# Kernel tuning notes

Measured on AMD Instinct MI355X. Metric: run time of the kernel, lower is better.

The kernel has to match this reference:

```python
import jax, jax.numpy as jnp
import numpy as np

NEG_SLOPE = 0.2
LN_EPS = 1e-5


def gat_conv(x, src, dst, n_nodes, W, a_src, a_dst, b, concat):
    # W: [F_in, H*C]; a_src, a_dst: [H, C]; b: [H*C] if concat else [C]
    H, C = a_src.shape
    h = (x @ W).reshape(-1, H, C)                      # [N, H, C]
    # per-node attention scores, gathered per edge
    s_src = jnp.einsum('nhc,hc->nh', h, a_src)          # [N, H]
    s_dst = jnp.einsum('nhc,hc->nh', h, a_dst)          # [N, H]
    e = jax.nn.leaky_relu(s_src[src] + s_dst[dst], NEG_SLOPE)  # [E, H]
    # segment softmax over incoming edges of each dst node
    e_max = jax.ops.segment_max(e, dst, num_segments=n_nodes)  # [N, H]
    w = jnp.exp(e - e_max[dst])
    denom = jax.ops.segment_sum(w, dst, num_segments=n_nodes)
    alpha = w / (denom[dst] + 1e-16)                    # [E, H]
    # weighted scatter-aggregate of source messages
    msg = h[src] * alpha[:, :, None]                    # [E, H, C]
    out = jax.ops.segment_sum(msg, dst, num_segments=n_nodes)  # [N, H, C]
    out = out.reshape(n_nodes, H * C) if concat else out.mean(axis=1)
    return out + b


def layer_norm(x, g, b):
    mu = x.mean(-1, keepdims=True)
    var = ((x - mu) ** 2).mean(-1, keepdims=True)
    return (x - mu) * jax.lax.rsqrt(var + LN_EPS) * g + b


def setup_inputs() -> dict:
    key = jax.random.key(0)
    ks = jax.random.split(key, 16)
    N, E, F_in = 50000, 400000, 128
    H1, C1 = 4, 128          # conv1: heads=4, hidden=128, concat -> 512
    C2 = 64                  # conv2: heads=1, out=64
    sd = lambda fan: 1.0 / np.sqrt(fan)
    inp = {
        'x': jax.random.normal(ks[0], (N, F_in), jnp.float32),
        'edge_index': jax.random.randint(ks[1], (2, E), 0, N, jnp.int64),
        'num_nodes': N,
        'W1': jax.random.normal(ks[2], (F_in, H1 * C1), jnp.float32) * sd(F_in),
        'a_src1': jax.random.normal(ks[3], (H1, C1), jnp.float32) * sd(C1),
        'a_dst1': jax.random.normal(ks[4], (H1, C1), jnp.float32) * sd(C1),
        'b1': jnp.zeros((H1 * C1,), jnp.float32),
        'W2': jax.random.normal(ks[5], (H1 * C1, C2), jnp.float32) * sd(H1 * C1),
        'a_src2': jax.random.normal(ks[6], (1, C2), jnp.float32) * sd(C2),
        'a_dst2': jax.random.normal(ks[7], (1, C2), jnp.float32) * sd(C2),
        'b2': jnp.zeros((C2,), jnp.float32),
        'Wm1': jax.random.normal(ks[8], (C2, 32), jnp.float32) * sd(C2),
        'bm1': jnp.zeros((32,), jnp.float32),
        'g_ln': jnp.ones((32,), jnp.float32),
        'b_ln': jnp.zeros((32,), jnp.float32),
        'Wm2': jax.random.normal(ks[9], (32, 16), jnp.float32) * sd(32),
        'bm2': jnp.zeros((16,), jnp.float32),
    }
    return inp


def reference(x, edge_index, num_nodes, W1, a_src1, a_dst1, b1, W2, a_src2, a_dst2, b2, Wm1, bm1, g_ln, b_ln, Wm2, bm2):
    N = num_nodes
    # PyG GATConv add_self_loops=True
    loop = jnp.arange(N, dtype=edge_index.dtype)
    src = jnp.concatenate([edge_index[0], loop])
    dst = jnp.concatenate([edge_index[1], loop])
    # dropout layers are identity in eval mode
    h = jax.nn.elu(gat_conv(x, src, dst, N, W1, a_src1, a_dst1, b1, concat=True))
    h = jax.nn.elu(gat_conv(h, src, dst, N, W2, a_src2, a_dst2, b2, concat=False))
    h = jax.nn.relu(layer_norm(h @ Wm1 + bm1, g_ln, b_ln))
    return h @ Wm2 + bm2  # [N, 2*n_spectral_dims]
```

## Files before the change

### kernel.cpp

```cpp
#include <hip/hip_runtime.h>
#include <cmath>


#define F_IN 128
#define H1   4
#define C1   128
#define D1   512
#define C2   64
#define DM1  32
#define DM2  16

#define LRELU(x) ((x) > 0.f ? (x) : 0.2f * (x))

typedef float f32x4 __attribute__((ext_vector_type(4)));
typedef short short8 __attribute__((ext_vector_type(8)));

static __device__ __forceinline__ float bf2f(unsigned short u) {
    return __builtin_bit_cast(float, (unsigned)u << 16);
}
static __device__ __forceinline__ unsigned short f2bf(float f) {
    unsigned u = __builtin_bit_cast(unsigned, f);
    u = (u + 0x7fffu + ((u >> 16) & 1u)) >> 16;
    return (unsigned short)u;
}

__global__ void k_detect(const void* ei, int E, int* flag) {
    __shared__ int any;
    if (threadIdx.x == 0) any = 0;
    __syncthreads();
    const int* p = (const int*)ei;
    int cnt = E < 4096 ? E : 4096;
    int stride = E / cnt;
    int local = 0;
    for (int i = threadIdx.x; i < cnt; i += blockDim.x) {
        long long idx = (long long)i * stride;
        local |= p[2 * idx + 1];
    }
    if (local) atomicOr(&any, 1);
    __syncthreads();
    if (threadIdx.x == 0) *flag = (any == 0) ? 1 : 0;
}

__global__ void k_convert(const void* ei, const int* flag, int E, int N,
                          int* src32, int* dst32, int* deg) {
    int i = blockIdx.x * blockDim.x + threadIdx.x;
    int Etot = E + N;
    if (i >= Etot) return;
    int s, d;
    if (i < E) {
        if (*flag) {
            const long long* q = (const long long*)ei;
            s = (int)q[i];
            d = (int)q[(size_t)E + i];
        } else {
            const int* q = (const int*)ei;
            s = q[i];
            d = q[(size_t)E + i];
        }
    } else {
        s = i - E;
        d = i - E;
    }
    src32[i] = s;
    dst32[i] = d;
    atomicAdd(&deg[d], 1);
}

__global__ __launch_bounds__(256) void k_scan1(const int* __restrict__ deg,
                                               int* __restrict__ bsum, int N) {
    int t = threadIdx.x;
    int base = blockIdx.x * 1024 + t * 4;
    int s = 0;
    if (base + 3 < N) {
        int4 v = *(const int4*)&deg[base];
        s = v.x + v.y + v.z + v.w;
    } else {
        for (int k = 0; k < 4; k++)
            if (base + k < N) s += deg[base + k];
    }
#pragma unroll
    for (int o = 1; o < 64; o <<= 1) s += __shfl_xor(s, o, 64);
    __shared__ int ws[4];
    if ((t & 63) == 0) ws[t >> 6] = s;
    __syncthreads();
    if (t == 0) bsum[blockIdx.x] = ws[0] + ws[1] + ws[2] + ws[3];
}

__global__ __launch_bounds__(1024) void k_scan2(const int* __restrict__ bsum,
                                                int* __restrict__ boff, int nb) {
    __shared__ int wsum[16];
    __shared__ int woff[16];
    int t = threadIdx.x, lane = t & 63, wid = t >> 6;
    int v = (t < nb) ? bsum[t] : 0;
    int x = v;
#pragma unroll
    for (int o = 1; o < 64; o <<= 1) {
        int tv = __shfl_up(x, o, 64);
        if (lane >= o) x += tv;
    }
    if (lane == 63) wsum[wid] = x;
    __syncthreads();
    if (wid == 0) {
        int y = (lane < 16) ? wsum[lane] : 0;
        int z = y;
#pragma unroll
        for (int o = 1; o < 16; o <<= 1) {
            int tv = __shfl_up(z, o, 64);
            if (lane >= o) z += tv;
        }
        if (lane < 16) woff[lane] = z - y;
    }
    __syncthreads();
    if (t < nb) boff[t] = woff[wid] + x - v;
}

__global__ __launch_bounds__(256) void k_scan3(const int* __restrict__ deg,
                                               const int* __restrict__ boff,
                                               int* __restrict__ rowstart,
                                               int* __restrict__ cursor, int N,
                                               int Etot) {
    int t = threadIdx.x, lane = t & 63, wid = t >> 6;
    int base = blockIdx.x * 1024 + t * 4;
    int v0 = 0, v1 = 0, v2 = 0, v3 = 0;
    if (base + 3 < N) {
        int4 v = *(const int4*)&deg[base];
        v0 = v.x; v1 = v.y; v2 = v.z; v3 = v.w;
    } else {
        if (base + 0 < N) v0 = deg[base + 0];
        if (base + 1 < N) v1 = deg[base + 1];
        if (base + 2 < N) v2 = deg[base + 2];
        if (base + 3 < N) v3 = deg[base + 3];
    }
    int s4 = v0 + v1 + v2 + v3;
    int x = s4;
#pragma unroll
    for (int o = 1; o < 64; o <<= 1) {
        int tv = __shfl_up(x, o, 64);
        if (lane >= o) x += tv;
    }
    __shared__ int ws[4];
    if (lane == 63) ws[wid] = x;
    __syncthreads();
    int woff = 0;
#pragma unroll
    for (int w = 0; w < 4; w++)
        if (w < wid) woff += ws[w];
    int ex = boff[blockIdx.x] + woff + (x - s4);
    int e0 = ex, e1 = ex + v0, e2 = e1 + v1, e3 = e2 + v2;
    if (base + 0 < N) { rowstart[base + 0] = e0; cursor[base + 0] = e0; }
    if (base + 1 < N) { rowstart[base + 1] = e1; cursor[base + 1] = e1; }
    if (base + 2 < N) { rowstart[base + 2] = e2; cursor[base + 2] = e2; }
    if (base + 3 < N) { rowstart[base + 3] = e3; cursor[base + 3] = e3; }
    if (blockIdx.x == 0 && t == 0) rowstart[N] = Etot;
}

__global__ void k_fill(const int* __restrict__ src32, const int* __restrict__ dst32,
                       int* __restrict__ cursor, int* __restrict__ adj, int Etot) {
    int i = blockIdx.x * blockDim.x + threadIdx.x;
    if (i < Etot) {
        int d = dst32[i];
        int pos = atomicAdd(&cursor[d], 1);
        adj[pos] = src32[i];
    }
}

__global__ void k_prep(const float* __restrict__ x, const float* __restrict__ W1,
                       const float* __restrict__ W2,
                       unsigned short* __restrict__ xb,
                       unsigned short* __restrict__ W1t,
                       unsigned short* __restrict__ W2t, int n8) {
    int i = blockIdx.x * blockDim.x + threadIdx.x;
    if (i < n8) {
        const float4* p = (const float4*)(x + (size_t)i * 8);
        float4 a = p[0], b = p[1];
        unsigned short r[8] = {f2bf(a.x), f2bf(a.y), f2bf(a.z), f2bf(a.w),
                               f2bf(b.x), f2bf(b.y), f2bf(b.z), f2bf(b.w)};
        *(short8*)(xb + (size_t)i * 8) = *(const short8*)r;
        return;
    }
    int i2 = i - n8;
    if (i2 < F_IN * D1) {
        int nn = i2 / F_IN, kk = i2 - nn * F_IN;
        W1t[i2] = f2bf(W1[(size_t)kk * D1 + nn]);
        return;
    }
    int i3 = i2 - F_IN * D1;
    if (i3 < D1 * C2) {
        int nn = i3 / D1, kk = i3 - nn * D1;
        W2t[i3] = f2bf(W2[(size_t)kk * C2 + nn]);
    }
}

template <int WM, int WN, int MF, int NF, bool OUT_BF16>
__global__ __launch_bounds__(256) void k_gemm_bf16(
    const unsigned short* __restrict__ A, const unsigned short* __restrict__ Bt,
    void* __restrict__ C, int M, int K, int NC) {
    constexpr int BM = WM * MF * 16;
    constexpr int BN = WN * NF * 16;
    constexpr int BK = 64;
    constexpr int LDK = BK + 8;
    __shared__ unsigned short As[BM][LDK];
    __shared__ unsigned short Bs[BN][LDK];
    const int tid = threadIdx.x;
    const int row0 = blockIdx.x * BM, col0 = blockIdx.y * BN;
    const int wave = tid >> 6, lane = tid & 63;
    const int wr = wave / WN, wc = wave % WN;
    const int lrow = lane & 15, lkg = lane >> 4;
    f32x4 acc[MF][NF] = {};
    for (int k0 = 0; k0 < K; k0 += BK) {
        for (int i = tid; i < BM * BK / 8; i += 256) {
            int r = i >> 3, kq = (i & 7) * 8;
            short8 v = {};
            if (row0 + r < M)
                v = *(const short8*)&A[(size_t)(row0 + r) * K + k0 + kq];
            *(short8*)&As[r][kq] = v;
        }
        for (int i = tid; i < BN * BK / 8; i += 256) {
            int r = i >> 3, kq = (i & 7) * 8;
            short8 v = *(const short8*)&Bt[(size_t)(col0 + r) * K + k0 + kq];
            *(short8*)&Bs[r][kq] = v;
        }
        __syncthreads();
#pragma unroll
        for (int kk = 0; kk < BK; kk += 32) {
            short8 af[MF], bfr[NF];
#pragma unroll
            for (int m = 0; m < MF; m++)
                af[m] = *(const short8*)&As[wr * MF * 16 + m * 16 + lrow][kk + lkg * 8];
#pragma unroll
            for (int n = 0; n < NF; n++)
                bfr[n] = *(const short8*)&Bs[wc * NF * 16 + n * 16 + lrow][kk + lkg * 8];
#pragma unroll
            for (int m = 0; m < MF; m++)
#pragma unroll
                for (int n = 0; n < NF; n++)
                    acc[m][n] = __builtin_amdgcn_mfma_f32_16x16x32_bf16(
                        af[m], bfr[n], acc[m][n], 0, 0, 0);
        }
        __syncthreads();
    }
#pragma unroll
    for (int m = 0; m < MF; m++)
#pragma unroll
        for (int n = 0; n < NF; n++)
#pragma unroll
            for (int r = 0; r < 4; r++) {
                int gr = row0 + wr * MF * 16 + m * 16 + lkg * 4 + r;
                int gc = col0 + wc * NF * 16 + n * 16 + lrow;
                if (gr < M) {
                    if (OUT_BF16)
                        ((unsigned short*)C)[(size_t)gr * NC + gc] = f2bf(acc[m][n][r]);
                    else
                        ((float*)C)[(size_t)gr * NC + gc] = acc[m][n][r];
                }
            }
}

__global__ void k_scores1(const unsigned short* __restrict__ h1b,
                          const float* __restrict__ a_src,
                          const float* __restrict__ a_dst,
                          float* __restrict__ s_src, float* __restrict__ s_dst,
                          int N) {
    int gid = blockIdx.x * blockDim.x + threadIdx.x;
    int n = gid >> 6, lane = gid & 63;
    if (n >= N) return;
    short8 hv = *(const short8*)&h1b[(size_t)n * D1 + lane * 8];
    float h[8];
#pragma unroll
    for (int j = 0; j < 8; j++) h[j] = bf2f((unsigned short)hv[j]);
    const float4* ap = (const float4*)&a_src[lane * 8];
    float4 a0 = ap[0], a1 = ap[1];
    const float4* bp = (const float4*)&a_dst[lane * 8];
    float4 b0 = bp[0], b1v = bp[1];
    float ss = h[0] * a0.x + h[1] * a0.y + h[2] * a0.z + h[3] * a0.w +
               h[4] * a1.x + h[5] * a1.y + h[6] * a1.z + h[7] * a1.w;
    float dd = h[0] * b0.x + h[1] * b0.y + h[2] * b0.z + h[3] * b0.w +
               h[4] * b1v.x + h[5] * b1v.y + h[6] * b1v.z + h[7] * b1v.w;
#pragma unroll
    for (int o = 1; o < 16; o <<= 1) {
        ss += __shfl_xor(ss, o, 64);
        dd += __shfl_xor(dd, o, 64);
    }
    if ((lane & 15) == 0) {
        int h4 = lane >> 4;
        s_src[(size_t)n * H1 + h4] = ss;
        s_dst[(size_t)n * H1 + h4] = dd;
    }
}

__global__ void k_scores2(const float* __restrict__ h2lin,
                          const float* __restrict__ a_src,
                          const float* __restrict__ a_dst,
                          float* __restrict__ s_src, float* __restrict__ s_dst,
                          int N) {
    int gid = blockIdx.x * blockDim.x + threadIdx.x;
    int n = gid >> 6, lane = gid & 63;
    if (n >= N) return;
    float v = h2lin[(size_t)n * C2 + lane];
    float ss = v * a_src[lane], dd = v * a_dst[lane];
#pragma unroll
    for (int o = 1; o < 64; o <<= 1) {
        ss += __shfl_xor(ss, o, 64);
        dd += __shfl_xor(dd, o, 64);
    }
    if (lane == 0) {
        s_src[n] = ss;
        s_dst[n] = dd;
    }
}

__global__ __launch_bounds__(256) void k_agg1(
    const unsigned short* __restrict__ h1b, const float* __restrict__ s_src,
    const float* __restrict__ s_dst, const int* __restrict__ rowstart,
    const int* __restrict__ adj, const float* __restrict__ b1,
    unsigned short* __restrict__ out1, int N) {
    int wv = (blockIdx.x * blockDim.x + threadIdx.x) >> 6;
    if (wv >= N) return;
    int lane = threadIdx.x & 63;
    int beg = rowstart[wv], end = rowstart[wv + 1];
    int h4 = lane & 3, jj = lane >> 2;
    float sdh = s_dst[(size_t)wv * 4 + h4];
    float m = -1e30f;
    for (int c0 = beg; c0 < end; c0 += 16) {
        int j = c0 + jj;
        if (j < end) {
            int sj = adj[j];
            float e = LRELU(s_src[(size_t)sj * 4 + h4] + sdh);
            m = fmaxf(m, e);
        }
    }
#pragma unroll
    for (int o = 4; o < 64; o <<= 1) m = fmaxf(m, __shfl_xor(m, o, 64));
    float dn = 0.f;
    for (int c0 = beg; c0 < end; c0 += 16) {
        int j = c0 + jj;
        if (j < end) {
            int sj = adj[j];
            float e = LRELU(s_src[(size_t)sj * 4 + h4] + sdh);
            dn += __expf(e - m);
        }
    }
#pragma unroll
    for (int o = 4; o < 64; o <<= 1) dn += __shfl_xor(dn, o, 64);
    float inv = 1.f / (dn + 1e-16f);
    int hg = lane >> 4;
    float mg = __shfl(m, hg, 64);
    float invg = __shfl(inv, hg, 64);
    float sdg = __shfl(sdh, hg, 64);
    float acc[8] = {};
    for (int j = beg; j < end; ++j) {
        int sj = adj[j];
        float e = LRELU(s_src[(size_t)sj * 4 + hg] + sdg);
        float a = __expf(e - mg) * invg;
        short8 v = *(const short8*)&h1b[(size_t)sj * D1 + lane * 8];
#pragma unroll
        for (int i = 0; i < 8; i++) acc[i] += a * bf2f((unsigned short)v[i]);
    }
    const float4* bp = (const float4*)&b1[lane * 8];
    float4 bb0 = bp[0], bb1 = bp[1];
    float r[8];
    r[0] = acc[0] + bb0.x; r[1] = acc[1] + bb0.y;
    r[2] = acc[2] + bb0.z; r[3] = acc[3] + bb0.w;
    r[4] = acc[4] + bb1.x; r[5] = acc[5] + bb1.y;
    r[6] = acc[6] + bb1.z; r[7] = acc[7] + bb1.w;
    unsigned short o16[8];
#pragma unroll
    for (int i = 0; i < 8; i++) {
        float z = r[i] > 0.f ? r[i] : expm1f(r[i]);
        o16[i] = f2bf(z);
    }
    *(short8*)&out1[(size_t)wv * D1 + lane * 8] = *(const short8*)o16;
}

__global__ __launch_bounds__(256) void k_agg2(
    const float* __restrict__ h2lin, const float* __restrict__ s_src,
    const float* __restrict__ s_dst, const int* __restrict__ rowstart,
    const int* __restrict__ adj, const float* __restrict__ b2,
    float* __restrict__ h2, int N) {
    int wv = (blockIdx.x * blockDim.x + threadIdx.x) >> 6;
    if (wv >= N) return;
    int lane = threadIdx.x & 63;
    int beg = rowstart[wv], end = rowstart[wv + 1];
    float sd = s_dst[wv];
    float m = -1e30f;
    for (int c0 = beg; c0 < end; c0 += 64) {
        int j = c0 + lane;
        if (j < end) m = fmaxf(m, LRELU(s_src[adj[j]] + sd));
    }
#pragma unroll
    for (int o = 1; o < 64; o <<= 1) m = fmaxf(m, __shfl_xor(m, o, 64));
    float dn = 0.f;
    for (int c0 = beg; c0 < end; c0 += 64) {
        int j = c0 + lane;
        if (j < end) dn += __expf(LRELU(s_src[adj[j]] + sd) - m);
    }
#pragma unroll
    for (int o = 1; o < 64; o <<= 1) dn += __shfl_xor(dn, o, 64);
    float inv = 1.f / (dn + 1e-16f);
    int eg = lane >> 4, ch = (lane & 15) * 4;
    float a0 = 0.f, a1 = 0.f, a2 = 0.f, a3 = 0.f;
    for (int j0 = beg; j0 < end; j0 += 4) {
        int j = j0 + eg;
        if (j < end) {
            int sj = adj[j];
            float a = __expf(LRELU(s_src[sj] + sd) - m) * inv;
            float4 r = *(const float4*)&h2lin[(size_t)sj * C2 + ch];
            a0 += a * r.x; a1 += a * r.y; a2 += a * r.z; a3 += a * r.w;
        }
    }
#pragma unroll
    for (int o = 16; o < 64; o <<= 1) {
        a0 += __shfl_xor(a0, o, 64);
        a1 += __shfl_xor(a1, o, 64);
        a2 += __shfl_xor(a2, o, 64);
        a3 += __shfl_xor(a3, o, 64);
    }
    if (lane < 16) {
        const float4 bb = *(const float4*)&b2[ch];
        float r0 = a0 + bb.x, r1 = a1 + bb.y, r2 = a2 + bb.z, r3 = a3 + bb.w;
        r0 = r0 > 0.f ? r0 : expm1f(r0);
        r1 = r1 > 0.f ? r1 : expm1f(r1);
        r2 = r2 > 0.f ? r2 : expm1f(r2);
        r3 = r3 > 0.f ? r3 : expm1f(r3);
        *(float4*)&h2[(size_t)wv * C2 + ch] = make_float4(r0, r1, r2, r3);
    }
}

__global__ __launch_bounds__(256) void k_mlp(
    const float* __restrict__ h2, const float* __restrict__ Wm1,
    const float* __restrict__ bm1, const float* __restrict__ g_ln,
    const float* __restrict__ b_ln, const float* __restrict__ Wm2,
    const float* __restrict__ bm2, float* __restrict__ out, int N) {
    __shared__ float w1[C2 * DM1];
    __shared__ float w2[DM1 * DM2];
    __shared__ float cb1[DM1], cg[DM1], cbl[DM1], cb2[DM2];
    int tid = threadIdx.x;
    for (int i = tid; i < C2 * DM1; i += 256) w1[i] = Wm1[i];
    for (int i = tid; i < DM1 * DM2; i += 256) w2[i] = Wm2[i];
    if (tid < DM1) {
        cb1[tid] = bm1[tid];
        cg[tid] = g_ln[tid];
        cbl[tid] = b_ln[tid];
    } else if (tid < DM1 + DM2) {
        cb2[tid - DM1] = bm2[tid - DM1];
    }
    __syncthreads();
    int n = blockIdx.x * 256 + tid;
    if (n >= N) return;
    float h[C2];
    const float4* hp = (const float4*)&h2[(size_t)n * C2];
#pragma unroll
    for (int i = 0; i < C2 / 4; i++) {
        float4 v = hp[i];
        h[4 * i] = v.x; h[4 * i + 1] = v.y;
        h[4 * i + 2] = v.z; h[4 * i + 3] = v.w;
    }
    float t[DM1];
#pragma unroll
    for (int j = 0; j < DM1; j++) {
        float a = cb1[j];
#pragma unroll
        for (int c = 0; c < C2; c++) a += h[c] * w1[c * DM1 + j];
        t[j] = a;
    }
    float mu = 0.f;
#pragma unroll
    for (int j = 0; j < DM1; j++) mu += t[j];
    mu *= (1.f / DM1);
    float var = 0.f;
#pragma unroll
    for (int j = 0; j < DM1; j++) {
        float d = t[j] - mu;
        var += d * d;
    }
    var *= (1.f / DM1);
    float rs = rsqrtf(var + 1e-5f);
#pragma unroll
    for (int j = 0; j < DM1; j++) {
        float z = (t[j] - mu) * rs * cg[j] + cbl[j];
        t[j] = z > 0.f ? z : 0.f;
    }
    float o[DM2];
#pragma unroll
    for (int k = 0; k < DM2; k++) {
        float a = cb2[k];
#pragma unroll
        for (int j = 0; j < DM1; j++) a += t[j] * w2[j * DM2 + k];
        o[k] = a;
    }
    float4* op = (float4*)&out[(size_t)n * DM2];
    op[0] = make_float4(o[0], o[1], o[2], o[3]);
    op[1] = make_float4(o[4], o[5], o[6], o[7]);
    op[2] = make_float4(o[8], o[9], o[10], o[11]);
    op[3] = make_float4(o[12], o[13], o[14], o[15]);
}

extern "C" void kernel_launch(void* const* d_in, const int* in_sizes, int n_in,
                              void* d_out, int out_size, void* d_ws,
                              size_t ws_size, hipStream_t stream) {
    const float* x      = (const float*)d_in[0];
    const void*  ei     = d_in[1];
    const float* W1     = (const float*)d_in[3];
    const float* a_src1 = (const float*)d_in[4];
    const float* a_dst1 = (const float*)d_in[5];
    const float* b1     = (const float*)d_in[6];
    const float* W2     = (const float*)d_in[7];
    const float* a_src2 = (const float*)d_in[8];
    const float* a_dst2 = (const float*)d_in[9];
    const float* b2     = (const float*)d_in[10];
    const float* Wm1    = (const float*)d_in[11];
    const float* bm1    = (const float*)d_in[12];
    const float* g_ln   = (const float*)d_in[13];
    const float* b_ln   = (const float*)d_in[14];
    const float* Wm2    = (const float*)d_in[15];
    const float* bm2    = (const float*)d_in[16];

    const int N    = in_sizes[0] / F_IN;
    const int E    = in_sizes[1] / 2;
    const int Etot = E + N;
    const int nb   = (N + 1023) / 1024;

    char* ws = (char*)d_ws;
    size_t off = 0;
    auto alloc = [&](size_t bytes) {
        size_t o = off;
        off += (bytes + 255) & ~(size_t)255;
        return o;
    };
    int*   flag     = (int*)(ws + alloc(4));
    int*   src32    = (int*)(ws + alloc((size_t)Etot * 4));
    int*   dst32    = (int*)(ws + alloc((size_t)Etot * 4));
    int*   deg      = (int*)(ws + alloc((size_t)N * 4));
    int*   bsum     = (int*)(ws + alloc(4096 * 4));
    int*   boff     = (int*)(ws + alloc(4096 * 4));
    int*   rowstart = (int*)(ws + alloc((size_t)(N + 1) * 4));
    int*   cursor   = (int*)(ws + alloc((size_t)N * 4));
    int*   adj      = (int*)(ws + alloc((size_t)Etot * 4));
    float* s_src1   = (float*)(ws + alloc((size_t)N * H1 * 4));
    float* s_dst1   = (float*)(ws + alloc((size_t)N * H1 * 4));
    unsigned short* xb   = (unsigned short*)(ws + alloc((size_t)N * F_IN * 2));
    unsigned short* W1t  = (unsigned short*)(ws + alloc((size_t)F_IN * D1 * 2));
    unsigned short* W2t  = (unsigned short*)(ws + alloc((size_t)D1 * C2 * 2));
    unsigned short* h1b  = (unsigned short*)(ws + alloc((size_t)N * D1 * 2));
    unsigned short* out1 = (unsigned short*)(ws + alloc((size_t)N * D1 * 2));
    float* h2lin = (float*)(ws + alloc((size_t)N * C2 * 4));
    float* h2    = (float*)(ws + alloc((size_t)N * C2 * 4));
    float* s_src2 = s_src1;
    float* s_dst2 = s_dst1;

    hipMemsetAsync(deg, 0, (size_t)N * 4, stream);
    k_detect<<<1, 256, 0, stream>>>(ei, E, flag);
    k_convert<<<(Etot + 255) / 256, 256, 0, stream>>>(ei, flag, E, N, src32, dst32, deg);
    k_scan1<<<nb, 256, 0, stream>>>(deg, bsum, N);
    k_scan2<<<1, 1024, 0, stream>>>(bsum, boff, nb);
    k_scan3<<<nb, 256, 0, stream>>>(deg, boff, rowstart, cursor, N, Etot);
    k_fill<<<(Etot + 255) / 256, 256, 0, stream>>>(src32, dst32, cursor, adj, Etot);

    int n8 = N * F_IN / 8;
    int prep_items = n8 + F_IN * D1 + D1 * C2;
    k_prep<<<(prep_items + 255) / 256, 256, 0, stream>>>(x, W1, W2, xb, W1t, W2t, n8);

    k_gemm_bf16<2, 2, 4, 4, true>
        <<<dim3((N + 127) / 128, D1 / 128), 256, 0, stream>>>(xb, W1t, h1b, N, F_IN, D1);
    k_scores1<<<((size_t)N * 64 + 255) / 256, 256, 0, stream>>>(h1b, a_src1, a_dst1,
                                                                s_src1, s_dst1, N);
    k_agg1<<<(N * 64 + 255) / 256, 256, 0, stream>>>(h1b, s_src1, s_dst1, rowstart,
                                                     adj, b1, out1, N);

    k_gemm_bf16<4, 1, 2, 4, false>
        <<<dim3((N + 127) / 128, 1), 256, 0, stream>>>(out1, W2t, h2lin, N, D1, C2);
    k_scores2<<<((size_t)N * 64 + 255) / 256, 256, 0, stream>>>(h2lin, a_src2, a_dst2,
                                                                s_src2, s_dst2, N);
    k_agg2<<<(N * 64 + 255) / 256, 256, 0, stream>>>(h2lin, s_src2, s_dst2, rowstart,
                                                     adj, b2, h2, N);

    k_mlp<<<(N + 255) / 256, 256, 0, stream>>>(h2, Wm1, bm1, g_ln, b_ln, Wm2, bm2,
                                               (float*)d_out, N);
}
```

Measured before the change: 374.8 us.

## Fuse attention-score dot products into GEMM epilogue and use direct-to-LDS swizzled loads

The per-node source and destination attention scores are now computed in the GEMM epilogue from the fp32 accumulators. Partial sums are reduced with cross-lane shuffles, then combined across waves through shared memory. This removes the separate scores kernels, their launches and their re-read of h1b and h2lin. Tile staging also switches to global_load_lds with an XOR-swizzled LDS layout instead of padded register-staged copies. The A-tile row bounds check is dropped, so the last partial tile reads past the end of A into adjacent workspace; layer-1 scores now use unrounded fp32 values rather than the bf16-rounded h1b.

```diff
diff --git a/kernel.cpp b/kernel.cpp
--- a/kernel.cpp
+++ b/kernel.cpp
@@ -191,16 +191,18 @@
     }
 }
 
-template <int WM, int WN, int MF, int NF, bool OUT_BF16>
+template <int WM, int WN, int MF, int NF, bool OUT_BF16, int SC_MODE>
 __global__ __launch_bounds__(256) void k_gemm_bf16(
     const unsigned short* __restrict__ A, const unsigned short* __restrict__ Bt,
-    void* __restrict__ C, int M, int K, int NC) {
+    void* __restrict__ C, int M, int K, int NC,
+    const float* __restrict__ avs, const float* __restrict__ avd,
+    float* __restrict__ s_src, float* __restrict__ s_dst) {
     constexpr int BM = WM * MF * 16;
     constexpr int BN = WN * NF * 16;
     constexpr int BK = 64;
-    constexpr int LDK = BK + 8;
-    __shared__ unsigned short As[BM][LDK];
-    __shared__ unsigned short Bs[BN][LDK];
+    __shared__ unsigned short As[BM * BK];
+    __shared__ unsigned short Bs[BN * BK];
+    __shared__ float ps_lds[WN][BM], pd_lds[WN][BM];
     const int tid = threadIdx.x;
     const int row0 = blockIdx.x * BM, col0 = blockIdx.y * BN;
     const int wave = tid >> 6, lane = tid & 63;
@@ -208,28 +210,42 @@
     const int lrow = lane & 15, lkg = lane >> 4;
     f32x4 acc[MF][NF] = {};
     for (int k0 = 0; k0 < K; k0 += BK) {
-        for (int i = tid; i < BM * BK / 8; i += 256) {
-            int r = i >> 3, kq = (i & 7) * 8;
-            short8 v = {};
-            if (row0 + r < M)
-                v = *(const short8*)&A[(size_t)(row0 + r) * K + k0 + kq];
-            *(short8*)&As[r][kq] = v;
-        }
-        for (int i = tid; i < BN * BK / 8; i += 256) {
-            int r = i >> 3, kq = (i & 7) * 8;
-            short8 v = *(const short8*)&Bt[(size_t)(col0 + r) * K + k0 + kq];
-            *(short8*)&Bs[r][kq] = v;
+#pragma unroll
+        for (int inst = 0; inst < (BM * 8) / 256; ++inst) {
+            int ibase = inst * 256 + wave * 64;
+            int i = ibase + lane;
+            int r = i >> 3, u = i & 7, su = u ^ (r & 7);
+            const unsigned short* gp = A + (size_t)(row0 + r) * K + k0 + su * 8;
+            __builtin_amdgcn_global_load_lds(
+                (const __attribute__((address_space(1))) void*)gp,
+                (__attribute__((address_space(3))) void*)&As[ibase * 8], 16, 0, 0);
+        }
+#pragma unroll
+        for (int inst = 0; inst < (BN * 8) / 256; ++inst) {
+            int ibase = inst * 256 + wave * 64;
+            int i = ibase + lane;
+            int r = i >> 3, u = i & 7, su = u ^ (r & 7);
+            const unsigned short* gp = Bt + (size_t)(col0 + r) * K + k0 + su * 8;
+            __builtin_amdgcn_global_load_lds(
+                (const __attribute__((address_space(1))) void*)gp,
+                (__attribute__((address_space(3))) void*)&Bs[ibase * 8], 16, 0, 0);
         }
         __syncthreads();
 #pragma unroll
         for (int kk = 0; kk < BK; kk += 32) {
             short8 af[MF], bfr[NF];
 #pragma unroll
-            for (int m = 0; m < MF; m++)
-                af[m] = *(const short8*)&As[wr * MF * 16 + m * 16 + lrow][kk + lkg * 8];
-#pragma unroll
-            for (int n = 0; n < NF; n++)
-                bfr[n] = *(const short8*)&Bs[wc * NF * 16 + n * 16 + lrow][kk + lkg * 8];
+            for (int m = 0; m < MF; m++) {
+                int ar = wr * MF * 16 + m * 16 + lrow;
+                int au = kk / 8 + lkg;
+                af[m] = *(const short8*)&As[(ar * 8 + (au ^ (lrow & 7))) * 8];
+            }
+#pragma unroll
+            for (int n = 0; n < NF; n++) {
+                int br = wc * NF * 16 + n * 16 + lrow;
+                int au = kk / 8 + lkg;
+                bfr[n] = *(const short8*)&Bs[(br * 8 + (au ^ (lrow & 7))) * 8];
+            }
 #pragma unroll
             for (int m = 0; m < MF; m++)
 #pragma unroll
@@ -254,58 +270,54 @@
                         ((float*)C)[(size_t)gr * NC + gc] = acc[m][n][r];
                 }
             }
-}
-
-__global__ void k_scores1(const unsigned short* __restrict__ h1b,
-                          const float* __restrict__ a_src,
-                          const float* __restrict__ a_dst,
-                          float* __restrict__ s_src, float* __restrict__ s_dst,
-                          int N) {
-    int gid = blockIdx.x * blockDim.x + threadIdx.x;
-    int n = gid >> 6, lane = gid & 63;
-    if (n >= N) return;
-    short8 hv = *(const short8*)&h1b[(size_t)n * D1 + lane * 8];
-    float h[8];
-#pragma unroll
-    for (int j = 0; j < 8; j++) h[j] = bf2f((unsigned short)hv[j]);
-    const float4* ap = (const float4*)&a_src[lane * 8];
-    float4 a0 = ap[0], a1 = ap[1];
-    const float4* bp = (const float4*)&a_dst[lane * 8];
-    float4 b0 = bp[0], b1v = bp[1];
-    float ss = h[0] * a0.x + h[1] * a0.y + h[2] * a0.z + h[3] * a0.w +
-               h[4] * a1.x + h[5] * a1.y + h[6] * a1.z + h[7] * a1.w;
-    float dd = h[0] * b0.x + h[1] * b0.y + h[2] * b0.z + h[3] * b0.w +
-               h[4] * b1v.x + h[5] * b1v.y + h[6] * b1v.z + h[7] * b1v.w;
-#pragma unroll
-    for (int o = 1; o < 16; o <<= 1) {
-        ss += __shfl_xor(ss, o, 64);
-        dd += __shfl_xor(dd, o, 64);
-    }
-    if ((lane & 15) == 0) {
-        int h4 = lane >> 4;
-        s_src[(size_t)n * H1 + h4] = ss;
-        s_dst[(size_t)n * H1 + h4] = dd;
-    }
-}
-
-__global__ void k_scores2(const float* __restrict__ h2lin,
-                          const float* __restrict__ a_src,
-                          const float* __restrict__ a_dst,
-                          float* __restrict__ s_src, float* __restrict__ s_dst,
-                          int N) {
-    int gid = blockIdx.x * blockDim.x + threadIdx.x;
-    int n = gid >> 6, lane = gid & 63;
-    if (n >= N) return;
-    float v = h2lin[(size_t)n * C2 + lane];
-    float ss = v * a_src[lane], dd = v * a_dst[lane];
-#pragma unroll
-    for (int o = 1; o < 64; o <<= 1) {
-        ss += __shfl_xor(ss, o, 64);
-        dd += __shfl_xor(dd, o, 64);
-    }
-    if (lane == 0) {
-        s_src[n] = ss;
-        s_dst[n] = dd;
+    if (SC_MODE) {
+        float asv[NF], adv[NF];
+#pragma unroll
+        for (int n = 0; n < NF; n++) {
+            int gc = col0 + wc * NF * 16 + n * 16 + lrow;
+            asv[n] = avs[gc];
+            adv[n] = avd[gc];
+        }
+#pragma unroll
+        for (int m = 0; m < MF; m++)
+#pragma unroll
+            for (int r = 0; r < 4; r++) {
+                float ps = 0.f, pd = 0.f;
+#pragma unroll
+                for (int n = 0; n < NF; n++) {
+                    ps += acc[m][n][r] * asv[n];
+                    pd += acc[m][n][r] * adv[n];
+                }
+#pragma unroll
+                for (int o = 1; o < 16; o <<= 1) {
+                    ps += __shfl_xor(ps, o, 64);
+                    pd += __shfl_xor(pd, o, 64);
+                }
+                if (lrow == 0) {
+                    int lr = wr * MF * 16 + m * 16 + lkg * 4 + r;
+                    ps_lds[wc][lr] = ps;
+                    pd_lds[wc][lr] = pd;
+                }
+            }
+        __syncthreads();
+        for (int rr = tid; rr < BM; rr += 256) {
+            int gr = row0 + rr;
+            if (gr < M) {
+                float s = 0.f, d = 0.f;
+#pragma unroll
+                for (int w = 0; w < WN; w++) {
+                    s += ps_lds[w][rr];
+                    d += pd_lds[w][rr];
+                }
+                if (SC_MODE == 1) {
+                    s_src[(size_t)gr * H1 + blockIdx.y] = s;
+                    s_dst[(size_t)gr * H1 + blockIdx.y] = d;
+                } else {
+                    s_src[gr] = s;
+                    s_dst[gr] = d;
+                }
+            }
+        }
     }
 }
 
@@ -560,17 +572,15 @@
     int prep_items = n8 + F_IN * D1 + D1 * C2;
     k_prep<<<(prep_items + 255) / 256, 256, 0, stream>>>(x, W1, W2, xb, W1t, W2t, n8);
 
-    k_gemm_bf16<2, 2, 4, 4, true>
-        <<<dim3((N + 127) / 128, D1 / 128), 256, 0, stream>>>(xb, W1t, h1b, N, F_IN, D1);
-    k_scores1<<<((size_t)N * 64 + 255) / 256, 256, 0, stream>>>(h1b, a_src1, a_dst1,
-                                                                s_src1, s_dst1, N);
+    k_gemm_bf16<2, 2, 4, 4, true, 1>
+        <<<dim3((N + 127) / 128, D1 / 128), 256, 0, stream>>>(
+            xb, W1t, h1b, N, F_IN, D1, a_src1, a_dst1, s_src1, s_dst1);
     k_agg1<<<(N * 64 + 255) / 256, 256, 0, stream>>>(h1b, s_src1, s_dst1, rowstart,
                                                      adj, b1, out1, N);
 
-    k_gemm_bf16<4, 1, 2, 4, false>
-        <<<dim3((N + 127) / 128, 1), 256, 0, stream>>>(out1, W2t, h2lin, N, D1, C2);
-    k_scores2<<<((size_t)N * 64 + 255) / 256, 256, 0, stream>>>(h2lin, a_src2, a_dst2,
-                                                                s_src2, s_dst2, N);
+    k_gemm_bf16<4, 1, 2, 4, false, 2>
+        <<<dim3((N + 127) / 128, 1), 256, 0, stream>>>(
+            out1, W2t, h2lin, N, D1, C2, a_src2, a_dst2, s_src2, s_dst2);
     k_agg2<<<(N * 64 + 255) / 256, 256, 0, stream>>>(h2lin, s_src2, s_dst2, rowstart,
                                                      adj, b2, h2, N);
 
```

Result: faster. 352.9 us (-5.8%).
